# Kernel tuning notes

Hardware: AMD Instinct MI355X
Metric: run time of the kernel (lower is better)

The kernel has to match this reference:

```python
import jax, jax.numpy as jnp
import numpy as np
import math

B, S, E, H, FF = 2, 2048, 768, 12, 3072
D = E // H
SCALING = 1.0
EPS = 1e-5


def layer_norm(x, g, b):
    mu = jnp.mean(x, axis=-1, keepdims=True)
    var = jnp.var(x, axis=-1, keepdims=True)
    return (x - mu) * jax.lax.rsqrt(var + EPS) * g + b


def setup_inputs() -> dict:
    key = jax.random.key(0)
    ks = jax.random.split(key, 16)
    s_e = 1.0 / math.sqrt(E)
    s_f = 1.0 / math.sqrt(FF)
    inp = {
        "x": jax.random.normal(ks[0], (B, S, E), dtype=jnp.float32),
        "Wq": jax.random.uniform(ks[1], (E, E), jnp.float32, -s_e, s_e),
        "bq": jnp.zeros((E,), jnp.float32),
        "Wk": jax.random.uniform(ks[2], (E, E), jnp.float32, -s_e, s_e),
        "bk": jnp.zeros((E,), jnp.float32),
        "Wv": jax.random.uniform(ks[3], (E, E), jnp.float32, -s_e, s_e),
        "bv": jnp.zeros((E,), jnp.float32),
        "Wo": jax.random.uniform(ks[4], (E, E), jnp.float32, -s_e, s_e),
        "bo": jnp.zeros((E,), jnp.float32),
        "W1": jax.random.uniform(ks[5], (E, FF), jnp.float32, -s_e, s_e),
        "b1": jnp.zeros((FF,), jnp.float32),
        "W2": jax.random.uniform(ks[6], (FF, E), jnp.float32, -s_f, s_f),
        "b2": jnp.zeros((E,), jnp.float32),
        "g1": jnp.ones((E,), jnp.float32),
        "be1": jnp.zeros((E,), jnp.float32),
        "g2": jnp.ones((E,), jnp.float32),
        "be2": jnp.zeros((E,), jnp.float32),
    }
    return inp


def reference(x, Wq, bq, Wk, bk, Wv, bv, Wo, bo, W1, b1, W2, b2, g1, be1, g2, be2):
    # --- multi-head attention with ALiBi-style symmetric distance bias ---
    q = (x @ Wq + bq).reshape(B, S, H, D)
    k = (x @ Wk + bk).reshape(B, S, H, D)
    v = (x @ Wv + bv).reshape(B, S, H, D)
    scores = jnp.einsum("bqhd,bkhd->bhqk", q, k) / math.sqrt(D)
    pos = jnp.arange(S)
    alibi = -SCALING * jnp.abs(pos[None, :] - pos[:, None]).astype(jnp.float32)  # [S,S]
    scores = scores + alibi  # broadcast over [B,H]
    attn_map = jax.nn.softmax(scores, axis=-1)  # [B,H,S,S]
    ctx = jnp.einsum("bhqk,bkhd->bqhd", attn_map, v).reshape(B, S, E)
    attn_out = ctx @ Wo + bo
    # --- residual + norm, FFN, residual + norm (dropout = eval/identity) ---
    h = layer_norm(x + attn_out, g1, be1)
    ff = jax.nn.relu(h @ W1 + b1) @ W2 + b2
    out = layer_norm(h + ff, g2, be2)
    return (out, attn_map)
```

## Files before the change

### kernel.cpp

```cpp
#include <hip/hip_runtime.h>
#include <stdint.h>

static constexpr int cB = 2, cS = 2048, cE = 768, cH = 12, cFF = 3072, cD = 64;
static constexpr int cM = cB * cS;

typedef __bf16 bf16x8 __attribute__((ext_vector_type(8)));
typedef float f32x4 __attribute__((ext_vector_type(4)));

__device__ __forceinline__ unsigned short f2bf(float f) {
    union { float f; unsigned int u; } v; v.f = f;
    unsigned int r = v.u + 0x7fffu + ((v.u >> 16) & 1u);
    return (unsigned short)(r >> 16);
}
__device__ __forceinline__ float bf2f(unsigned short u) {
    union { unsigned int u; float f; } v; v.u = ((unsigned int)u) << 16;
    return v.f;
}

__device__ __forceinline__ void load_lds16(const unsigned short* g, unsigned short* l) {
    __builtin_amdgcn_global_load_lds(
        (const __attribute__((address_space(1))) unsigned int*)(g),
        (__attribute__((address_space(3))) unsigned int*)(l), 16, 0, 0);
}

static constexpr int ZJOBS_PER_BLOCK = 12288;

template<int BM, int BN, int EPI>
__global__ __launch_bounds__(256, 4) void gemm_nt(
    const unsigned short* __restrict__ Ab,
    const unsigned short* __restrict__ Btp,
    float* __restrict__ outF,
    float* __restrict__ outF2,
    unsigned short* __restrict__ outB,
    unsigned short* __restrict__ outB2,
    const float* __restrict__ bias0,
    const float* __restrict__ bias1,
    const float* __restrict__ bias2,
    const float* __restrict__ resid,
    float* __restrict__ zattn, int zbase,
    int M, int N, int K, long sB)
{
    constexpr int MI = BM / 32, NI = BN / 32;
    __shared__ alignas(16) unsigned short Sh[BM * 64 + BN * 64];
    unsigned short* Al = Sh;
    unsigned short* Bl = Sh + BM * 64;
    const int tid = threadIdx.x;
    const int lane = tid & 63, wave = tid >> 6;
    const int wm = wave >> 1, wn = wave & 1;
    const int bz = blockIdx.z;
    const int m0 = blockIdx.y * BM, n0 = blockIdx.x * BN;
    const int ln = lane & 15, lg = lane >> 4;
    const int sw = ln & 7;

    const unsigned short* Bt = Btp + (size_t)bz * sB;

    f32x4 acc[MI][NI];
#pragma unroll
    for (int i = 0; i < MI; i++)
#pragma unroll
        for (int j = 0; j < NI; j++) acc[i][j] = (f32x4){0.f, 0.f, 0.f, 0.f};

    int kbeg = 0, kend = K;
    if constexpr (EPI == 3) { int kh = K >> 1; kbeg = bz * kh; kend = kbeg + kh; }

    for (int k0 = kbeg; k0 < kend; k0 += 64) {
        __syncthreads();
#pragma unroll
        for (int it = 0; it < BM / 32; ++it) {
            int idx = tid + it * 256;
            int r = idx >> 3, c8 = idx & 7;
            int cs = c8 ^ (r & 7);
            load_lds16(Ab + (size_t)(m0 + r) * K + k0 + cs * 8, &Al[idx * 8]);
        }
#pragma unroll
        for (int it = 0; it < BN / 32; ++it) {
            int idx = tid + it * 256;
            int r = idx >> 3, c8 = idx & 7;
            int cs = c8 ^ (r & 7);
            load_lds16(Bt + (size_t)(n0 + r) * K + k0 + cs * 8, &Bl[idx * 8]);
        }
        __syncthreads();
#pragma unroll
        for (int ks = 0; ks < 2; ++ks) {
            bf16x8 av[MI], bv[NI];
#pragma unroll
            for (int i = 0; i < MI; i++) {
                int row = wm * (BM / 2) + 16 * i + ln;
                av[i] = *(const bf16x8*)&Al[row * 64 + ((ks * 4 + lg) ^ sw) * 8];
            }
#pragma unroll
            for (int j = 0; j < NI; j++) {
                int row = wn * (BN / 2) + 16 * j + ln;
                bv[j] = *(const bf16x8*)&Bl[row * 64 + ((ks * 4 + lg) ^ sw) * 8];
            }
#pragma unroll
            for (int i = 0; i < MI; i++)
#pragma unroll
                for (int j = 0; j < NI; j++)
                    acc[i][j] = __builtin_amdgcn_mfma_f32_16x16x32_bf16(av[i], bv[j], acc[i][j], 0, 0, 0);
        }
    }

    if constexpr (EPI == 3 || EPI == 4) {
        const int lin = blockIdx.x + gridDim.x * (blockIdx.y + gridDim.y * blockIdx.z);
        const size_t zb = (size_t)(zbase + lin) * ZJOBS_PER_BLOCK;
        const f32x4 z4 = {0.f, 0.f, 0.f, 0.f};
        f32x4* zp = (f32x4*)zattn;
        for (int jj = tid; jj < ZJOBS_PER_BLOCK; jj += 256) {
            size_t j = zb + jj;
            int row  = (int)(j >> 9);
            int slot = (int)(j & 511);
            int m064 = (row & 2047) & ~63;
            int ntlo = (m064 > 120) ? ((m064 - 120) >> 7) : 0;
            int nthi = (m064 + 183) >> 7; nthi = nthi > 15 ? 15 : nthi;
            int zlo = ntlo << 5;
            int span = ((nthi + 1) << 5) - zlo;
            int chunk = slot < zlo ? slot : slot + span;
            if (chunk < 512)
                __builtin_nontemporal_store(z4, zp + ((size_t)row << 9) + chunk);
        }
    }

    if constexpr (EPI == 0) {
        if (bz < 2) {
            const float* bia = (bz == 0) ? bias0 : bias1;
#pragma unroll
            for (int i = 0; i < MI; i++)
#pragma unroll
                for (int j = 0; j < NI; j++)
#pragma unroll
                    for (int r = 0; r < 4; r++) {
                        int m = m0 + wm * (BM / 2) + 16 * i + lg * 4 + r;
                        int n = n0 + wn * (BN / 2) + 16 * j + ln;
                        float v = acc[i][j][r] + bia[n];
                        int b = m >> 11, s = m & 2047, h = n >> 6, d = n & 63;
                        outB[(size_t)bz * ((size_t)cB * cH * cS * cD) +
                             ((((size_t)b * cH + h) * cS + s) << 6) + d] = f2bf(v);
                    }
        } else {
            constexpr int TS = BM + 8;
            __syncthreads();
#pragma unroll
            for (int i = 0; i < MI; i++)
#pragma unroll
                for (int j = 0; j < NI; j++)
#pragma unroll
                    for (int r = 0; r < 4; r++) {
                        int ml = wm * (BM / 2) + 16 * i + lg * 4 + r;
                        int nl = wn * (BN / 2) + 16 * j + ln;
                        Sh[nl * TS + ml] = f2bf(acc[i][j][r] + bias2[n0 + nl]);
                    }
            __syncthreads();
            const int b = m0 >> 11, sbase = m0 & 2047;
#pragma unroll
            for (int it = 0; it < (BN * BM / 8) / 256; ++it) {
                int idx = tid + it * 256;
                int rr = idx >> 4, c8 = idx & 15;
                uint4 val = *(const uint4*)&Sh[rr * TS + c8 * 8];
                int ng = n0 + rr;
                int h = ng >> 6, d = ng & 63;
                *(uint4*)&outB2[((((size_t)b * cH + h) << 6) + d) * (size_t)cS + sbase + c8 * 8] = val;
            }
        }
    } else if constexpr (EPI == 3) {
        float* o = (bz == 0) ? outF : outF2;
#pragma unroll
        for (int i = 0; i < MI; i++) {
#pragma unroll
            for (int j = 0; j < NI; j++) {
#pragma unroll
                for (int r = 0; r < 4; r++) {
                    int m = m0 + wm * (BM / 2) + 16 * i + lg * 4 + r;
                    int n = n0 + wn * (BN / 2) + 16 * j + ln;
                    float v = acc[i][j][r];
                    if (bz == 0) v += bias0[n] + resid[(size_t)m * N + n];
                    o[(size_t)m * N + n] = v;
                }
            }
        }
    } else {
#pragma unroll
        for (int i = 0; i < MI; i++) {
#pragma unroll
            for (int j = 0; j < NI; j++) {
#pragma unroll
                for (int r = 0; r < 4; r++) {
                    int m = m0 + wm * (BM / 2) + 16 * i + lg * 4 + r;
                    int n = n0 + wn * (BN / 2) + 16 * j + ln;
                    float v = fmaxf(acc[i][j][r] + bias0[n], 0.f);
                    outB[(size_t)m * N + n] = f2bf(v);
                }
            }
        }
    }
}

__global__ __launch_bounds__(256, 2) void attn_fused(
    const unsigned short* __restrict__ Qh,
    const unsigned short* __restrict__ Kh,
    const unsigned short* __restrict__ Vt,
    float* __restrict__ attn,
    unsigned short* __restrict__ ctxb)
{
    constexpr int VS = 136;
    __shared__ alignas(16) unsigned short KVl[128 * 64];
    __shared__ alignas(16) unsigned short Pl[3 * 64 * VS];
    __shared__ float rs2[2][64];
    __shared__ float rsinv[64];

    const int tid = threadIdx.x;
    const int lane = tid & 63, wave = tid >> 6;
    const int wm = wave >> 1, wn = wave & 1;
    const int ln = lane & 15, lg = lane >> 4;
    const int sw = ln & 7;
    const int m0 = blockIdx.x * 64;
    const int bh = blockIdx.y;

    const int nt_lo = max(0, (m0 - 120) / 128);
    const int nt_hi = min(15, (m0 + 183) / 128);

    const unsigned short* Qg = Qh + ((size_t)bh * cS + m0) * cD;
    const unsigned short* Kg = Kh + (size_t)bh * cS * cD;
    const unsigned short* Vg = Vt + (size_t)bh * cD * cS;
    float* attng = attn + (size_t)bh * cS * cS;

#pragma unroll
    for (int it = 0; it < 2; ++it) {
        int idx = tid + it * 256;
        int r = idx >> 3, c8 = idx & 7;
        int cs = c8 ^ (r & 7);
        load_lds16(Qg + r * cD + cs * 8, &KVl[idx * 8]);
    }
    __syncthreads();
    bf16x8 qf[2][2];
#pragma unroll
    for (int ks = 0; ks < 2; ++ks)
#pragma unroll
        for (int i = 0; i < 2; i++)
            qf[ks][i] = *(const bf16x8*)&KVl[(wm * 32 + 16 * i + ln) * 64 + ((ks * 4 + lg) ^ sw) * 8];

    float psum[8];
#pragma unroll
    for (int k = 0; k < 8; k++) psum[k] = 0.f;
    f32x4 oacc[2][2];
#pragma unroll
    for (int i = 0; i < 2; i++)
#pragma unroll
        for (int j = 0; j < 2; j++) oacc[i][j] = (f32x4){0.f, 0.f, 0.f, 0.f};

    for (int nt = nt_lo; nt <= nt_hi; ++nt) {
        unsigned short* Pb = &Pl[(nt - nt_lo) * 64 * VS];
        __syncthreads();
#pragma unroll
        for (int it = 0; it < 4; ++it) {
            int idx = tid + it * 256;
            int r = idx >> 3, c8 = idx & 7;
            int cs = c8 ^ (r & 7);
            load_lds16(Kg + (size_t)(nt * 128 + r) * cD + cs * 8, &KVl[idx * 8]);
        }
        __syncthreads();
        f32x4 acc[2][4];
#pragma unroll
        for (int i = 0; i < 2; i++)
#pragma unroll
            for (int j = 0; j < 4; j++) acc[i][j] = (f32x4){0.f, 0.f, 0.f, 0.f};
#pragma unroll
        for (int ks = 0; ks < 2; ++ks) {
            bf16x8 b[4];
#pragma unroll
            for (int j = 0; j < 4; j++)
                b[j] = *(const bf16x8*)&KVl[(wn * 64 + 16 * j + ln) * 64 + ((ks * 4 + lg) ^ sw) * 8];
            __builtin_amdgcn_s_setprio(1);
#pragma unroll
            for (int i = 0; i < 2; i++)
#pragma unroll
                for (int j = 0; j < 4; j++)
                    acc[i][j] = __builtin_amdgcn_mfma_f32_16x16x32_bf16(qf[ks][i], b[j], acc[i][j], 0, 0, 0);
            __builtin_amdgcn_s_setprio(0);
        }
#pragma unroll
        for (int i = 0; i < 2; i++)
#pragma unroll
            for (int j = 0; j < 4; j++)
#pragma unroll
                for (int r = 0; r < 4; r++) {
                    int mloc = wm * 32 + 16 * i + lg * 4 + r;
                    int nloc = wn * 64 + 16 * j + ln;
                    int mg = m0 + mloc, ng = nt * 128 + nloc;
                    float e = __expf(acc[i][j][r] * 0.125f - fabsf((float)(mg - ng)));
                    psum[i * 4 + r] += e;
                    Pb[mloc * VS + nloc] = f2bf(e);
                }
        __syncthreads();
#pragma unroll
        for (int it = 0; it < 4; ++it) {
            int idx = tid + it * 256;
            int r = idx >> 4, c8 = idx & 15;
            int cs = c8 ^ (r & 7);
            load_lds16(Vg + (size_t)r * cS + nt * 128 + cs * 8, &KVl[idx * 8]);
        }
        __syncthreads();
#pragma unroll
        for (int ks = 0; ks < 4; ++ks) {
            bf16x8 pa[2], vb[2];
#pragma unroll
            for (int i = 0; i < 2; i++)
                pa[i] = *(const bf16x8*)&Pb[(wm * 32 + 16 * i + ln) * VS + ks * 32 + lg * 8];
#pragma unroll
            for (int j = 0; j < 2; j++) {
                int row = wn * 32 + 16 * j + ln;
                vb[j] = *(const bf16x8*)&KVl[row * 128 + ((ks * 4 + lg) ^ sw) * 8];
            }
            __builtin_amdgcn_s_setprio(1);
#pragma unroll
            for (int i = 0; i < 2; i++)
#pragma unroll
                for (int j = 0; j < 2; j++)
                    oacc[i][j] = __builtin_amdgcn_mfma_f32_16x16x32_bf16(pa[i], vb[j], oacc[i][j], 0, 0, 0);
            __builtin_amdgcn_s_setprio(0);
        }
    }

#pragma unroll
    for (int k = 0; k < 8; k++) {
        float v = psum[k];
        v += __shfl_xor(v, 1); v += __shfl_xor(v, 2);
        v += __shfl_xor(v, 4); v += __shfl_xor(v, 8);
        psum[k] = v;
    }
    if (ln == 0) {
#pragma unroll
        for (int i = 0; i < 2; i++)
#pragma unroll
            for (int r = 0; r < 4; r++)
                rs2[wn][wm * 32 + 16 * i + lg * 4 + r] = psum[i * 4 + r];
    }
    __syncthreads();
    if (tid < 64) rsinv[tid] = 1.f / (rs2[0][tid] + rs2[1][tid]);
    __syncthreads();
    float invl[8];
#pragma unroll
    for (int i = 0; i < 2; i++)
#pragma unroll
        for (int r = 0; r < 4; r++)
            invl[i * 4 + r] = rsinv[wm * 32 + 16 * i + lg * 4 + r];

    {
        int b = bh / cH, h = bh % cH;
#pragma unroll
        for (int i = 0; i < 2; i++)
#pragma unroll
            for (int j = 0; j < 2; j++)
#pragma unroll
                for (int r = 0; r < 4; r++) {
                    int mg = m0 + wm * 32 + 16 * i + lg * 4 + r;
                    int d = wn * 32 + 16 * j + ln;
                    ctxb[((size_t)b * cS + mg) * cE + h * 64 + d] = f2bf(oacc[i][j][r] * invl[i * 4 + r]);
                }
    }
    for (int nt = nt_lo; nt <= nt_hi; ++nt) {
        const unsigned short* Pb = &Pl[(nt - nt_lo) * 64 * VS];
#pragma unroll
        for (int t = 0; t < 8; ++t) {
            int idx = t * 256 + tid;
            int row = idx >> 5, c4 = idx & 31;
            ushort4 pv = *(const ushort4*)&Pb[row * VS + c4 * 4];
            float s = rsinv[row];
            float4 o;
            o.x = bf2f(pv.x) * s; o.y = bf2f(pv.y) * s;
            o.z = bf2f(pv.z) * s; o.w = bf2f(pv.w) * s;
            *(float4*)&attng[(size_t)(m0 + row) * cS + nt * 128 + c4 * 4] = o;
        }
    }
}

template<bool WH, bool TWO>
__global__ __launch_bounds__(256) void layernorm_k(const float* __restrict__ in,
    const float* __restrict__ in2,
    const float* __restrict__ g, const float* __restrict__ be,
    float* __restrict__ outF, unsigned short* __restrict__ outB)
{
    const size_t row = blockIdx.x;
    const float* p = in + row * cE;
    const int tid = threadIdx.x;
    float x0 = p[tid], x1 = p[tid + 256], x2 = p[tid + 512];
    if constexpr (TWO) {
        const float* q = in2 + row * cE;
        x0 += q[tid]; x1 += q[tid + 256]; x2 += q[tid + 512];
    }
    float sum = x0 + x1 + x2, sq = x0 * x0 + x1 * x1 + x2 * x2;
    __shared__ float s1[4], s2[4];
    for (int o = 32; o; o >>= 1) { sum += __shfl_xor(sum, o); sq += __shfl_xor(sq, o); }
    if ((tid & 63) == 0) { s1[tid >> 6] = sum; s2[tid >> 6] = sq; }
    __syncthreads();
    sum = s1[0] + s1[1] + s1[2] + s1[3];
    sq  = s2[0] + s2[1] + s2[2] + s2[3];
    float mu = sum * (1.f / cE);
    float var = sq * (1.f / cE) - mu * mu;
    float rstd = rsqrtf(var + 1e-5f);
#pragma unroll
    for (int i = 0; i < 3; i++) {
        int c = tid + 256 * i;
        float xv = (i == 0) ? x0 : ((i == 1) ? x1 : x2);
        float y = (xv - mu) * rstd * g[c] + be[c];
        outF[row * cE + c] = y;
        if constexpr (WH) outB[row * cE + c] = f2bf(y);
    }
}

__global__ __launch_bounds__(256) void prep_all(
    const float* __restrict__ x, unsigned short* __restrict__ xb,
    const float* __restrict__ Wq, const float* __restrict__ Wk,
    const float* __restrict__ Wv, const float* __restrict__ Wo,
    const float* __restrict__ W1, const float* __restrict__ W2,
    unsigned short* __restrict__ Wqt, unsigned short* __restrict__ W1t,
    unsigned short* __restrict__ W2t)
{
    __shared__ float t[32][33];
    int bid = blockIdx.x;
    if (bid < 3072) {
        int i = bid * 256 + threadIdx.x;
        float4 v = ((const float4*)x)[i];
        ushort4 o;
        o.x = f2bf(v.x); o.y = f2bf(v.y); o.z = f2bf(v.z); o.w = f2bf(v.w);
        ((ushort4*)xb)[i] = o;
        return;
    }
    bid -= 3072;
    const float* src; unsigned short* dst; int R, C, tx, ty;
    if (bid < 2304) {
        int m = bid / 576, tt = bid - m * 576;
        src = (m == 0) ? Wq : (m == 1) ? Wk : (m == 2) ? Wv : Wo;
        dst = Wqt + (size_t)m * 589824;
        R = 768; C = 768; tx = tt % 24; ty = tt / 24;
    } else if (bid < 4608) {
        int tt = bid - 2304;
        src = W1; dst = W1t; R = 768; C = 3072; tx = tt % 96; ty = tt / 96;
    } else {
        int tt = bid - 4608;
        src = W2; dst = W2t; R = 3072; C = 768; tx = tt % 24; ty = tt / 24;
    }
    int c0 = tx * 32, r0 = ty * 32;
    int lx = threadIdx.x & 31, ly = threadIdx.x >> 5;
#pragma unroll
    for (int i = 0; i < 32; i += 8) t[ly + i][lx] = src[(size_t)(r0 + ly + i) * C + c0 + lx];
    __syncthreads();
#pragma unroll
    for (int i = 0; i < 32; i += 8) dst[(size_t)(c0 + ly + i) * R + r0 + lx] = f2bf(t[lx][ly + i]);
}

extern "C" void kernel_launch(void* const* d_in, const int* in_sizes, int n_in,
                              void* d_out, int out_size, void* d_ws, size_t ws_size,
                              hipStream_t stream)
{
    const float* x   = (const float*)d_in[0];
    const float* Wq  = (const float*)d_in[1];
    const float* bq  = (const float*)d_in[2];
    const float* Wk  = (const float*)d_in[3];
    const float* bk  = (const float*)d_in[4];
    const float* Wv  = (const float*)d_in[5];
    const float* bv  = (const float*)d_in[6];
    const float* Wo  = (const float*)d_in[7];
    const float* bo  = (const float*)d_in[8];
    const float* W1  = (const float*)d_in[9];
    const float* b1  = (const float*)d_in[10];
    const float* W2  = (const float*)d_in[11];
    const float* b2  = (const float*)d_in[12];
    const float* g1  = (const float*)d_in[13];
    const float* be1 = (const float*)d_in[14];
    const float* g2  = (const float*)d_in[15];
    const float* be2 = (const float*)d_in[16];

    float* out  = (float*)d_out;
    float* attn = out + (size_t)cB * cS * cE;

    char* ws = (char*)d_ws;
    unsigned short* xb   = (unsigned short*)(ws + 0);
    unsigned short* ctxb = xb;
    unsigned short* Wqt  = (unsigned short*)(ws + 6291456);
    unsigned short* W1t  = (unsigned short*)(ws + 11010048);
    unsigned short* W2t  = (unsigned short*)(ws + 15728640);
    unsigned short* Qh   = (unsigned short*)(ws + 20447232);
    unsigned short* Kh   = (unsigned short*)(ws + 26738688);
    unsigned short* Vt   = (unsigned short*)(ws + 33030144);
    unsigned short* ff1b = Qh;
    float* res1a = (float*)(ws + 45613056);
    float* res1b = (float*)(ws + 58195968);
    float* hf    = res1a;
    float* res2a = (float*)(ws + 58195968);
    float* res2b = (float*)(ws + 0);
    unsigned short* hb = (unsigned short*)(ws + 70778880);

    prep_all<<<9984, 256, 0, stream>>>(x, xb, Wq, Wk, Wv, Wo, W1, W2, Wqt, W1t, W2t);
    gemm_nt<128, 96, 0><<<dim3(8, 32, 3), 256, 0, stream>>>(
        xb, Wqt, nullptr, nullptr, Qh, Vt, bq, bk, bv, nullptr, nullptr, 0,
        cM, cE, cE, 589824);
    attn_fused<<<dim3(cS / 64, cB * cH), 256, 0, stream>>>(Qh, Kh, Vt, attn, ctxb);
    gemm_nt<128, 96, 3><<<dim3(8, 32, 2), 256, 0, stream>>>(
        ctxb, Wqt + 3 * 589824, res1a, res1b, nullptr, nullptr, bo, nullptr, nullptr, x,
        attn, 0, cM, cE, cE, 0);
    layernorm_k<true, true><<<cM, 256, 0, stream>>>(res1a, res1b, g1, be1, hf, hb);
    gemm_nt<128, 96, 4><<<dim3(32, 32, 1), 256, 0, stream>>>(
        hb, W1t, nullptr, nullptr, ff1b, nullptr, b1, nullptr, nullptr, nullptr,
        attn, 512, cM, cFF, cE, 0);
    gemm_nt<128, 96, 3><<<dim3(8, 32, 2), 256, 0, stream>>>(
        ff1b, W2t, res2a, res2b, nullptr, nullptr, b2, nullptr, nullptr, hf,
        attn, 1536, cM, cE, cFF, 0);
    layernorm_k<false, true><<<cM, 256, 0, stream>>>(res2a, res2b, g2, be2, out, nullptr);
}
```

Baseline: 598.8 us.

## Interleave attention-map zero stores into GEMM K-loops across all GEMMs

The zero-fill of the off-band attention map entries was previously done in the epilogue of three GEMMs. It is now spread over four GEMMs, including the QKV projection, in smaller per-block chunks. A few store batches are issued inside each K-loop iteration so the nontemporal writes overlap MFMA work instead of forming a serial tail. Any chunks not yet written are flushed after the loop. This adds a runtime branch and address math inside the main loop and may compete with the LDS loads for memory bandwidth.

```diff
diff --git a/kernel.cpp b/kernel.cpp
--- a/kernel.cpp
+++ b/kernel.cpp
@@ -23,7 +23,9 @@
         (__attribute__((address_space(3))) unsigned int*)(l), 16, 0, 0);
 }
 
-static constexpr int ZJOBS_PER_BLOCK = 12288;
+static constexpr size_t ZTOT = 25165824;
+static constexpr int ZPB = 9216;
+static constexpr int ZPT = 36;
 
 template<int BM, int BN, int EPI>
 __global__ __launch_bounds__(256, 4) void gemm_nt(
@@ -37,7 +39,7 @@
     const float* __restrict__ bias1,
     const float* __restrict__ bias2,
     const float* __restrict__ resid,
-    float* __restrict__ zattn, int zbase,
+    float* __restrict__ zattn, int zbase, int zqs,
     int M, int N, int K, long sB)
 {
     constexpr int MI = BM / 32, NI = BN / 32;
@@ -54,6 +56,11 @@
 
     const unsigned short* Bt = Btp + (size_t)bz * sB;
 
+    const int lin = blockIdx.x + gridDim.x * (blockIdx.y + gridDim.y * blockIdx.z);
+    const size_t zb = (size_t)(zbase + lin) * ZPB;
+    int zq0 = 0;
+    const f32x4 z4 = {0.f, 0.f, 0.f, 0.f};
+
     f32x4 acc[MI][NI];
 #pragma unroll
     for (int i = 0; i < MI; i++)
@@ -99,25 +106,40 @@
                 for (int j = 0; j < NI; j++)
                     acc[i][j] = __builtin_amdgcn_mfma_f32_16x16x32_bf16(av[i], bv[j], acc[i][j], 0, 0, 0);
         }
-    }
-
-    if constexpr (EPI == 3 || EPI == 4) {
-        const int lin = blockIdx.x + gridDim.x * (blockIdx.y + gridDim.y * blockIdx.z);
-        const size_t zb = (size_t)(zbase + lin) * ZJOBS_PER_BLOCK;
-        const f32x4 z4 = {0.f, 0.f, 0.f, 0.f};
-        f32x4* zp = (f32x4*)zattn;
-        for (int jj = tid; jj < ZJOBS_PER_BLOCK; jj += 256) {
-            size_t j = zb + jj;
-            int row  = (int)(j >> 9);
-            int slot = (int)(j & 511);
-            int m064 = (row & 2047) & ~63;
-            int ntlo = (m064 > 120) ? ((m064 - 120) >> 7) : 0;
-            int nthi = (m064 + 183) >> 7; nthi = nthi > 15 ? 15 : nthi;
-            int zlo = ntlo << 5;
-            int span = ((nthi + 1) << 5) - zlo;
-            int chunk = slot < zlo ? slot : slot + span;
-            if (chunk < 512)
-                __builtin_nontemporal_store(z4, zp + ((size_t)row << 9) + chunk);
+        if (zattn) {
+            for (int q = 0; q < zqs && (zq0 + q) < ZPT; ++q) {
+                size_t j = zb + (size_t)(zq0 + q) * 256 + tid;
+                if (j < ZTOT) {
+                    int row  = (int)(j >> 9);
+                    int slot = (int)(j & 511);
+                    int m064 = (row & 2047) & ~63;
+                    int ntlo = (m064 > 120) ? ((m064 - 120) >> 7) : 0;
+                    int nthi = (m064 + 183) >> 7; if (nthi > 15) nthi = 15;
+                    int zlo = ntlo << 5;
+                    int span = ((nthi + 1) << 5) - zlo;
+                    int chunk = slot < zlo ? slot : slot + span;
+                    if (chunk < 512)
+                        __builtin_nontemporal_store(z4, (f32x4*)zattn + ((size_t)row << 9) + chunk);
+                }
+            }
+            zq0 += zqs;
+        }
+    }
+    if (zattn) {
+        for (; zq0 < ZPT; ++zq0) {
+            size_t j = zb + (size_t)zq0 * 256 + tid;
+            if (j < ZTOT) {
+                int row  = (int)(j >> 9);
+                int slot = (int)(j & 511);
+                int m064 = (row & 2047) & ~63;
+                int ntlo = (m064 > 120) ? ((m064 - 120) >> 7) : 0;
+                int nthi = (m064 + 183) >> 7; if (nthi > 15) nthi = 15;
+                int zlo = ntlo << 5;
+                int span = ((nthi + 1) << 5) - zlo;
+                int chunk = slot < zlo ? slot : slot + span;
+                if (chunk < 512)
+                    __builtin_nontemporal_store(z4, (f32x4*)zattn + ((size_t)row << 9) + chunk);
+            }
         }
     }
 
@@ -493,18 +515,18 @@
 
     prep_all<<<9984, 256, 0, stream>>>(x, xb, Wq, Wk, Wv, Wo, W1, W2, Wqt, W1t, W2t);
     gemm_nt<128, 96, 0><<<dim3(8, 32, 3), 256, 0, stream>>>(
-        xb, Wqt, nullptr, nullptr, Qh, Vt, bq, bk, bv, nullptr, nullptr, 0,
+        xb, Wqt, nullptr, nullptr, Qh, Vt, bq, bk, bv, nullptr, attn, 0, 3,
         cM, cE, cE, 589824);
     attn_fused<<<dim3(cS / 64, cB * cH), 256, 0, stream>>>(Qh, Kh, Vt, attn, ctxb);
     gemm_nt<128, 96, 3><<<dim3(8, 32, 2), 256, 0, stream>>>(
         ctxb, Wqt + 3 * 589824, res1a, res1b, nullptr, nullptr, bo, nullptr, nullptr, x,
-        attn, 0, cM, cE, cE, 0);
+        attn, 768, 6, cM, cE, cE, 0);
     layernorm_k<true, true><<<cM, 256, 0, stream>>>(res1a, res1b, g1, be1, hf, hb);
     gemm_nt<128, 96, 4><<<dim3(32, 32, 1), 256, 0, stream>>>(
         hb, W1t, nullptr, nullptr, ff1b, nullptr, b1, nullptr, nullptr, nullptr,
-        attn, 512, cM, cFF, cE, 0);
+        attn, 1280, 3, cM, cFF, cE, 0);
     gemm_nt<128, 96, 3><<<dim3(8, 32, 2), 256, 0, stream>>>(
         ff1b, W2t, res2a, res2b, nullptr, nullptr, b2, nullptr, nullptr, hf,
-        attn, 1536, cM, cE, cFF, 0);
+        attn, 2304, 2, cM, cE, cFF, 0);
     layernorm_k<false, true><<<cM, 256, 0, stream>>>(res2a, res2b, g2, be2, out, nullptr);
 }
```

New measurement: 582.1 us. 2.8% less time.
